# Performance work log

Measured on AMD Instinct MI355X. Metric: run time of the kernel, lower is better.

The kernel has to match this reference:

```python
import jax, jax.numpy as jnp
import numpy as np

L = 2          # num_hidden_layers
B = 8          # max_batch_size
H = 8          # num_kv_heads_per_rank
S = 4096       # sequence_length (max cache len)
D = 128        # head_dim


def setup_inputs() -> dict:
    key = jax.random.key(0)
    k1, k2, k3 = jax.random.split(key, 3)
    kv_cache = jax.random.normal(k1, (2 * L, B, H, S, D), dtype=jnp.float32)
    new_kv = jax.random.normal(k2, (L, 2, B, H, 1, D), dtype=jnp.float32)
    position_ids = jax.random.randint(k3, (B, 1), 0, S, dtype=jnp.int64)
    return {"kv_cache": kv_cache, "new_kv": new_kv, "position_ids": position_ids}


def reference(kv_cache, new_kv, position_ids):
    """Token-generation KV cache update (right padding, no flash decoding).

    Equivalent to, per layer:
      scatter_index_new = position_ids.view(-1,1,1,1).expand_as(latest_k)
      k_cache = torch.scatter(k_cache, dim=2, index=scatter_index_new, src=latest_k)
      v_cache = torch.scatter(v_cache, dim=2, index=scatter_index_new, src=latest_v)
    """
    b_idx = jnp.arange(kv_cache.shape[1])            # (B,)
    pos = position_ids[:, 0]                          # (B,)
    outs = []
    for l in range(new_kv.shape[0]):
        latest_k = new_kv[l, 0, :, :, 0, :]           # (B, H, D)
        latest_v = new_kv[l, 1, :, :, 0, :]           # (B, H, D)
        # advanced indices (b_idx, pos) separated by ':' -> selects (B, H, D)
        k_upd = kv_cache[2 * l].at[b_idx, :, pos, :].set(latest_k)
        v_upd = kv_cache[2 * l + 1].at[b_idx, :, pos, :].set(latest_v)
        outs.append(k_upd)
        outs.append(v_upd)
    return jnp.stack(outs)                            # (2L, B, H, S, D)
```

## Files before the change

### kernel.cpp

```cpp
#include <hip/hip_runtime.h>


#define LL 2
#define BB 8
#define HH 8
#define SS 4096
#define DD 128

__global__ void kv_scatter_kernel(const float4* __restrict__ new_kv,
                                  const int* __restrict__ pos_ids,
                                  float* __restrict__ out) {
    int tid = blockIdx.x * blockDim.x + threadIdx.x;
    int d4   = tid & (DD / 4 - 1);
    int rest = tid >> 5;
    int h    = rest & (HH - 1);
    rest >>= 3;
    int b    = rest & (BB - 1);
    int c    = rest >> 3;
    int pos  = pos_ids[b];

    float4 v = new_kv[tid];
    size_t row = ((((size_t)c * BB + b) * HH + h) * SS + (size_t)pos);
    float4* dst = (float4*)(out + row * DD) + d4;
    *dst = v;
}

extern "C" void kernel_launch(void* const* d_in, const int* in_sizes, int n_in,
                              void* d_out, int out_size, void* d_ws, size_t ws_size,
                              hipStream_t stream) {
    const float* kv_cache = (const float*)d_in[0];
    const float* new_kv   = (const float*)d_in[1];
    const int*   pos_ids  = (const int*)d_in[2];
    float*       out      = (float*)d_out;

    size_t bytes = (size_t)out_size * sizeof(float);
    hipMemcpyAsync(d_out, (const void*)kv_cache, bytes,
                   hipMemcpyDeviceToDevice, stream);

    const int total_f4 = LL * 2 * BB * HH * (DD / 4);
    const int block = 256;
    kv_scatter_kernel<<<total_f4 / block, block, 0, stream>>>(
        (const float4*)new_kv, pos_ids, out);
}
```

Measured before the change: 852.2 us.

## Fuse cache copy and token scatter into one grid-stride kernel

Replaces the device-to-device memcpy plus separate scatter kernel with a single grid-stride kernel. It streams the whole cache with nontemporal loads and stores, substituting the new token row wherever the sequence index matches the position. This removes one launch and the separate copy pass, and may beat the runtime's copy engine or blit kernel. The cost is a per-element position check and a fixed grid size.

```diff
diff --git a/kernel.cpp b/kernel.cpp
--- a/kernel.cpp
+++ b/kernel.cpp
@@ -7,38 +7,40 @@
 #define SS 4096
 #define DD 128
 
-__global__ void kv_scatter_kernel(const float4* __restrict__ new_kv,
-                                  const int* __restrict__ pos_ids,
-                                  float* __restrict__ out) {
-    int tid = blockIdx.x * blockDim.x + threadIdx.x;
-    int d4   = tid & (DD / 4 - 1);
-    int rest = tid >> 5;
-    int h    = rest & (HH - 1);
-    rest >>= 3;
-    int b    = rest & (BB - 1);
-    int c    = rest >> 3;
-    int pos  = pos_ids[b];
+typedef float f32x4 __attribute__((ext_vector_type(4)));
 
-    float4 v = new_kv[tid];
-    size_t row = ((((size_t)c * BB + b) * HH + h) * SS + (size_t)pos);
-    float4* dst = (float4*)(out + row * DD) + d4;
-    *dst = v;
+#define TOTAL_F4 (2 * LL * BB * HH * SS * (DD / 4))
+
+__global__ __launch_bounds__(256) void kv_copy_scatter(
+    const f32x4* __restrict__ cache,
+    const f32x4* __restrict__ new_kv,
+    const int*   __restrict__ pos_ids,
+    f32x4*       __restrict__ out)
+{
+    const int stride = gridDim.x * blockDim.x;
+    int i = blockIdx.x * blockDim.x + threadIdx.x;
+    for (; i < TOTAL_F4; i += stride) {
+        f32x4 v = __builtin_nontemporal_load(&cache[i]);
+        int s = (i >> 5)  & (SS - 1);
+        int b = (i >> 20) & (BB - 1);
+        int pos = pos_ids[b];
+        if (s == pos) {
+            int d4 = i & (DD / 4 - 1);
+            int h  = (i >> 17) & (HH - 1);
+            int c  = i >> 23;
+            v = new_kv[((c * BB + b) * HH + h) * (DD / 4) + d4];
+        }
+        __builtin_nontemporal_store(v, &out[i]);
+    }
 }
 
 extern "C" void kernel_launch(void* const* d_in, const int* in_sizes, int n_in,
                               void* d_out, int out_size, void* d_ws, size_t ws_size,
                               hipStream_t stream) {
-    const float* kv_cache = (const float*)d_in[0];
-    const float* new_kv   = (const float*)d_in[1];
+    const f32x4* kv_cache = (const f32x4*)d_in[0];
+    const f32x4* new_kv   = (const f32x4*)d_in[1];
     const int*   pos_ids  = (const int*)d_in[2];
-    float*       out      = (float*)d_out;
+    f32x4*       out      = (f32x4*)d_out;
 
-    size_t bytes = (size_t)out_size * sizeof(float);
-    hipMemcpyAsync(d_out, (const void*)kv_cache, bytes,
-                   hipMemcpyDeviceToDevice, stream);
-
-    const int total_f4 = LL * 2 * BB * HH * (DD / 4);
-    const int block = 256;
-    kv_scatter_kernel<<<total_f4 / block, block, 0, stream>>>(
-        (const float4*)new_kv, pos_ids, out);
+    kv_copy_scatter<<<2048, 256, 0, stream>>>(kv_cache, new_kv, pos_ids, out);
 }
```

After: 852.5 us. Within noise of the previous version (+0.0%).
